# Kernel optimization log

Measured on AMD Instinct MI355X. Metric: run time of the kernel, lower is better.

Reference implementation:

```python
import jax, jax.numpy as jnp
import numpy as np

N = 20000
E = 640000
IN_CH = 256
HID = 128
OUT_CH = 64
HEADS = 8
C1 = HID // HEADS   # 16 per-head dim, layer 1 (concat)
C2 = OUT_CH         # 64 per-head dim, layer 2 (head mean)
NEG_SLOPE = 0.2


def gat_conv(x, edge_index, W, a_src, a_dst, b, concat):
    """PyG GATConv (no self loops, eval mode / no dropout).
    W: [F_in, H*C], a_src/a_dst: [H, C], b: [H*C] or [C]."""
    H, C = a_src.shape
    h = (x @ W).reshape(-1, H, C)                      # [N, H, C]
    s_src = jnp.einsum('nhc,hc->nh', h, a_src)         # [N, H]
    s_dst = jnp.einsum('nhc,hc->nh', h, a_dst)         # [N, H]
    src, dst = edge_index[0], edge_index[1]
    e = jax.nn.leaky_relu(s_src[src] + s_dst[dst], NEG_SLOPE)  # [E, H]
    # segment softmax over incoming edges of each destination node
    m = jax.ops.segment_max(e, dst, num_segments=N)    # [N, H] (-inf for isolated)
    p = jnp.exp(e - m[dst])                            # [E, H]
    z = jax.ops.segment_sum(p, dst, num_segments=N)    # [N, H]
    alpha = p / z[dst]                                 # [E, H]
    out = jax.ops.segment_sum(h[src] * alpha[..., None], dst, num_segments=N)  # [N,H,C]
    out = out.reshape(-1, H * C) if concat else out.mean(axis=1)
    return out + b


def hetero_layer(x, edge_indices, Ws, a_srcs, a_dsts, bs, concat):
    # HeteroConv(aggr='mean') over edge types targeting 'user'
    outs = [gat_conv(x, edge_indices[t], Ws[t], a_srcs[t], a_dsts[t], bs[t], concat)
            for t in range(len(edge_indices))]
    return sum(outs) / len(outs)


def setup_inputs() -> dict:
    key = jax.random.key(0)
    ks = jax.random.split(key, 16)
    g = 0.1
    return {
        'x': jax.random.normal(ks[0], (N, IN_CH), dtype=jnp.float32),
        'edge_index_a': jax.random.randint(ks[1], (2, E), 0, N, dtype=jnp.int32).astype(jnp.int64),
        'edge_index_b': jax.random.randint(ks[2], (2, E), 0, N, dtype=jnp.int32).astype(jnp.int64),
        # layer 1 params, stacked over 2 edge types
        'W1': jax.random.normal(ks[3], (2, IN_CH, HEADS * C1), dtype=jnp.float32) * g,
        'a1_src': jax.random.normal(ks[4], (2, HEADS, C1), dtype=jnp.float32) * g,
        'a1_dst': jax.random.normal(ks[5], (2, HEADS, C1), dtype=jnp.float32) * g,
        'b1': jnp.zeros((2, HEADS * C1), dtype=jnp.float32),
        # layer 2 params
        'W2': jax.random.normal(ks[6], (2, HID, HEADS * C2), dtype=jnp.float32) * g,
        'a2_src': jax.random.normal(ks[7], (2, HEADS, C2), dtype=jnp.float32) * g,
        'a2_dst': jax.random.normal(ks[8], (2, HEADS, C2), dtype=jnp.float32) * g,
        'b2': jnp.zeros((2, C2), dtype=jnp.float32),
        # classifier
        'Wc1': jax.random.normal(ks[9], (OUT_CH, 32), dtype=jnp.float32) * g,
        'bc1': jnp.zeros((32,), dtype=jnp.float32),
        'Wc2': jax.random.normal(ks[10], (32, 2), dtype=jnp.float32) * g,
        'bc2': jnp.zeros((2,), dtype=jnp.float32),
    }


def reference(x, edge_index_a, edge_index_b, W1, a1_src, a1_dst, b1,
              W2, a2_src, a2_dst, b2, Wc1, bc1, Wc2, bc2):
    eis = [edge_index_a, edge_index_b]
    h = hetero_layer(x, eis, W1, a1_src, a1_dst, b1, concat=True)   # [N, 128]
    h = jax.nn.elu(h)  # (dropout is identity in eval mode)
    h = hetero_layer(h, eis, W2, a2_src, a2_dst, b2, concat=False)  # [N, 64]
    h = jax.nn.elu(h)
    logits = jax.nn.relu(h @ Wc1 + bc1) @ Wc2 + bc2                 # [N, 2]
    return logits
```

## Files before the change

### kernel.cpp

```cpp
#include <hip/hip_runtime.h>
#include <hip/hip_bf16.h>
#include <math.h>

#define NN 20000
#define EE 640000
#define NB 157
#define BCAP 5120
#define NBLK 160
#define CHNK 4000

typedef float v2f __attribute__((ext_vector_type(2)));

__device__ __forceinline__ void wave_fence() {
  __builtin_amdgcn_wave_barrier();
  asm volatile("s_waitcnt lgkmcnt(0)" ::: "memory");
  __builtin_amdgcn_wave_barrier();
}

__device__ __forceinline__ unsigned pack_bf2(float a, float b) {
  __hip_bfloat162 h2 = __float22bfloat162_rn(make_float2(a, b));
  return *(unsigned*)&h2;
}
__device__ __forceinline__ float2 unpack_bf2(unsigned v) {
  float2 r;
  unsigned lo = v << 16, hi = v & 0xffff0000u;
  r.x = __uint_as_float(lo);
  r.y = __uint_as_float(hi);
  return r;
}

__global__ __launch_bounds__(256) void bin_k(const int* __restrict__ ea,
                                             const int* __restrict__ eb,
                                             int* __restrict__ gcnt,
                                             int* __restrict__ bbuf) {
  int t = blockIdx.y;
  const int* ei = t ? eb : ea;
  int tid = threadIdx.x;
  __shared__ int lh[NB], lbase[NB];
  if (tid < NB) lh[tid] = 0;
  __syncthreads();
  int e0 = blockIdx.x * CHNK;
  int e1 = min(e0 + CHNK, EE);
  int myb[16], myr[16], myv[16];
#pragma unroll
  for (int i = 0; i < 16; ++i) {
    int e = e0 + tid + i * 256;
    if (e < e1) {
      int s = ei[e], d = ei[EE + e];
      int b = d >> 7;
      myb[i] = b;
      myv[i] = (s << 7) | (d & 127);
      myr[i] = atomicAdd(&lh[b], 1);
    } else {
      myb[i] = -1;
    }
  }
  __syncthreads();
  if (tid < NB) {
    int c = lh[tid];
    lbase[tid] = c ? atomicAdd(&gcnt[t * NB + tid], c) : 0;
  }
  __syncthreads();
#pragma unroll
  for (int i = 0; i < 16; ++i) {
    int b = myb[i];
    if (b >= 0) {
      int pos = lbase[b] + myr[i];
      if (pos < BCAP) bbuf[((size_t)t * NB + b) * BCAP + pos] = myv[i];
    }
  }
}

__global__ __launch_bounds__(512) void bscan_k(const int* __restrict__ gcnt,
                                               int* __restrict__ bstart) {
  __shared__ int buf[512];
  int tid = threadIdx.x;
  int t = tid >> 8, b = tid & 255;
  int val = (b < NB) ? gcnt[t * NB + b] : 0;
  buf[tid] = val;
  __syncthreads();
  for (int s = 1; s < 256; s <<= 1) {
    int x = ((tid & 255) >= s) ? buf[tid - s] : 0;
    __syncthreads();
    buf[tid] += x;
    __syncthreads();
  }
  if (b < NB) bstart[t * NB + b] = buf[tid] - val;
}

__global__ __launch_bounds__(256) void build_k(const int* __restrict__ gcnt,
                                               const int* __restrict__ bstart,
                                               const int* __restrict__ bbuf,
                                               int* __restrict__ rowptr,
                                               int* __restrict__ csr) {
  int b = blockIdx.x, t = blockIdx.y;
  int cnt = gcnt[t * NB + b];
  int start = bstart[t * NB + b];
  int n0 = b << 7;
  int nlocal = min(128, NN - n0);
  int tid = threadIdx.x;
  __shared__ int arr[128], lcur[128];
  if (tid < 128) arr[tid] = 0;
  __syncthreads();
  const int* ebuf = bbuf + ((size_t)t * NB + b) * BCAP;
  for (int i = tid; i < cnt; i += 256) atomicAdd(&arr[ebuf[i] & 127], 1);
  __syncthreads();
  int deg = (tid < 128) ? arr[tid] : 0;
  for (int s = 1; s < 128; s <<= 1) {
    int x = (tid < 128 && tid >= s) ? arr[tid - s] : 0;
    __syncthreads();
    if (tid < 128) arr[tid] += x;
    __syncthreads();
  }
  if (tid < nlocal) {
    int incl = arr[tid];
    rowptr[t * (NN + 1) + n0 + tid + 1] = start + incl;
    lcur[tid] = start + incl - deg;
  }
  if (b == 0 && tid == 0) rowptr[t * (NN + 1)] = 0;
  __syncthreads();
  for (int i = tid; i < cnt; i += 256) {
    int v = ebuf[i];
    int pos = atomicAdd(&lcur[v & 127], 1);
    csr[(size_t)t * EE + pos] = v >> 7;
  }
}

template <int NT, int BM, int BN, int BK, int TM, int TN>
__global__ __launch_bounds__(NT) void sgemm_k(const float* __restrict__ A,
                                              const float* __restrict__ B,
                                              float* __restrict__ C, int M, int N, int K,
                                              long long Abs, long long Bbs, long long Cbs,
                                              unsigned* __restrict__ Cb, long long Cbb) {
  A += blockIdx.z * Abs; B += blockIdx.z * Bbs; C += blockIdx.z * Cbs;
  if (Cb) Cb += blockIdx.z * Cbb;
  const int bm = blockIdx.x * BM, bn = blockIdx.y * BN;
  __shared__ float As[BK][BM + 4];
  __shared__ float Bs[BK][BN + 4];
  int tid = threadIdx.x;
  constexpr int TX = BN / TN;
  int tx = tid % TX, ty = tid / TX;
  float acc[TM][TN] = {};
  for (int k0 = 0; k0 < K; k0 += BK) {
#pragma unroll
    for (int i = 0; i < (BM * BK) / (NT * 4); ++i) {
      int idx = tid + i * NT;
      int row = idx / (BK / 4), kq = idx % (BK / 4);
      float4 v = make_float4(0.f, 0.f, 0.f, 0.f);
      int gr = bm + row;
      if (gr < M) v = *(const float4*)&A[(size_t)gr * K + k0 + kq * 4];
      As[kq * 4 + 0][row] = v.x; As[kq * 4 + 1][row] = v.y;
      As[kq * 4 + 2][row] = v.z; As[kq * 4 + 3][row] = v.w;
    }
#pragma unroll
    for (int i = 0; i < (BK * BN) / (NT * 4); ++i) {
      int idx = tid + i * NT;
      int row = idx / (BN / 4), cq = idx % (BN / 4);
      *(float4*)&Bs[row][cq * 4] = *(const float4*)&B[(size_t)(k0 + row) * N + bn + cq * 4];
    }
    __syncthreads();
#pragma unroll
    for (int k = 0; k < BK; ++k) {
      float a[TM], b[TN];
#pragma unroll
      for (int i = 0; i < TM; i += 4) *(float4*)&a[i] = *(float4*)&As[k][ty * TM + i];
#pragma unroll
      for (int j = 0; j < TN; j += 4) *(float4*)&b[j] = *(float4*)&Bs[k][tx * TN + j];
#pragma unroll
      for (int i = 0; i < TM; ++i)
#pragma unroll
        for (int j = 0; j < TN; ++j) acc[i][j] += a[i] * b[j];
    }
    __syncthreads();
  }
#pragma unroll
  for (int i = 0; i < TM; ++i) {
    int gr = bm + ty * TM + i;
    if (gr < M) {
#pragma unroll
      for (int j = 0; j < TN; j += 4)
        *(float4*)&C[(size_t)gr * N + bn + tx * TN + j] = *(float4*)&acc[i][j];
      if (Cb) {
#pragma unroll
        for (int j = 0; j < TN; j += 2)
          Cb[(size_t)gr * (N >> 1) + ((bn + tx * TN + j) >> 1)] = pack_bf2(acc[i][j], acc[i][j + 1]);
      }
    }
  }
}

template <int NT, int BM, int BK, int TM, int TN, int KC>
__global__ __launch_bounds__(NT) void sgemm_splitk_k(const unsigned* __restrict__ Ap,
                                                     const float* __restrict__ B,
                                                     float* __restrict__ P, int M, int K) {
  const int N = 64;
  int t = blockIdx.z;
  Ap += (size_t)t * M * (K >> 1);
  B += (size_t)t * 65536;
  P += ((size_t)t * 4 + blockIdx.y) * M * N;
  const int bm = blockIdx.x * BM;
  const int k0base = blockIdx.y * KC;
  __shared__ float As[BK][BM + 4];
  __shared__ float Bs[BK][N + 4];
  int tid = threadIdx.x;
  constexpr int TX = N / TN;
  int tx = tid % TX, ty = tid / TX;
  float acc[TM][TN] = {};
  for (int k0 = k0base; k0 < k0base + KC; k0 += BK) {
    {
      int row = tid >> 2, q = tid & 3;
      int gr = bm + row;
      uint4 u = make_uint4(0u, 0u, 0u, 0u);
      if (gr < M) u = *(const uint4*)&Ap[(size_t)gr * (K >> 1) + (k0 >> 1) + q * 4];
      float2 f0 = unpack_bf2(u.x), f1 = unpack_bf2(u.y);
      float2 f2 = unpack_bf2(u.z), f3 = unpack_bf2(u.w);
      int kl = q * 8;
      As[kl + 0][row] = f0.x; As[kl + 1][row] = f0.y;
      As[kl + 2][row] = f1.x; As[kl + 3][row] = f1.y;
      As[kl + 4][row] = f2.x; As[kl + 5][row] = f2.y;
      As[kl + 6][row] = f3.x; As[kl + 7][row] = f3.y;
    }
#pragma unroll
    for (int i = 0; i < (BK * N) / (NT * 4); ++i) {
      int idx = tid + i * NT;
      int row = idx / (N / 4), cq = idx % (N / 4);
      *(float4*)&Bs[row][cq * 4] = *(const float4*)&B[(size_t)(k0 + row) * N + cq * 4];
    }
    __syncthreads();
#pragma unroll
    for (int k = 0; k < BK; ++k) {
      float a[TM], b[TN];
#pragma unroll
      for (int i = 0; i < TM; i += 4) *(float4*)&a[i] = *(float4*)&As[k][ty * TM + i];
#pragma unroll
      for (int j = 0; j < TN; j += 4) *(float4*)&b[j] = *(float4*)&Bs[k][tx * TN + j];
#pragma unroll
      for (int i = 0; i < TM; ++i)
#pragma unroll
        for (int j = 0; j < TN; ++j) acc[i][j] += a[i] * b[j];
    }
    __syncthreads();
  }
#pragma unroll
  for (int i = 0; i < TM; ++i) {
    int gr = bm + ty * TM + i;
    if (gr < M) {
#pragma unroll
      for (int j = 0; j < TN; j += 4)
        *(float4*)&P[(size_t)gr * N + tx * TN + j] = *(float4*)&acc[i][j];
    }
  }
}

template <int C>
__global__ void score_k(const float* __restrict__ hf, const float* __restrict__ as_,
                        const float* __restrict__ ad_, float* __restrict__ ss,
                        float* __restrict__ sd) {
  int idx = blockIdx.x * 256 + threadIdx.x;
  if (idx >= 2 * NN * 8) return;
  int t = idx / (NN * 8), r = idx % (NN * 8), n = r / 8, hh = r % 8;
  const int HC = 8 * C;
  const float* hrow = hf + (size_t)t * NN * HC + (size_t)n * HC + hh * C;
  const float* a1 = as_ + t * HC + hh * C;
  const float* a2 = ad_ + t * HC + hh * C;
  float s1 = 0.f, s2 = 0.f;
#pragma unroll
  for (int c = 0; c < C; c += 4) {
    float4 f = *(const float4*)&hrow[c];
    float4 u = *(const float4*)&a1[c];
    float4 w = *(const float4*)&a2[c];
    s1 += f.x * u.x + f.y * u.y + f.z * u.z + f.w * u.w;
    s2 += f.x * w.x + f.y * w.y + f.z * w.z + f.w * w.w;
  }
  ss[idx] = s1; sd[idx] = s2;
}

__device__ __forceinline__ float lrelu(float v) { return v > 0.f ? v : 0.2f * v; }

__global__ __launch_bounds__(256) void aggw1_k(const int* __restrict__ rowptr,
                                               const int* __restrict__ csr,
                                               const float* __restrict__ ssrc,
                                               const float* __restrict__ sdst,
                                               const unsigned* __restrict__ hb,
                                               float* __restrict__ out) {
  int t = blockIdx.y;
  rowptr += t * (NN + 1); csr += (size_t)t * EE;
  ssrc += (size_t)t * NN * 8; sdst += (size_t)t * NN * 8;
  hb += (size_t)t * NN * 64; out += (size_t)t * NN * 128;
  int tid = threadIdx.x, w = tid >> 6, lane = tid & 63;
  int n = blockIdx.x * 4 + w;
  int row = rowptr[n], end = rowptr[n + 1];
  __shared__ int sidx[4][64];
  __shared__ float sexp[4][64][8];
  float4 sda = *(const float4*)&sdst[(size_t)n * 8];
  float4 sdb = *(const float4*)&sdst[(size_t)n * 8 + 4];
  float za_x = 0.f, za_y = 0.f, za_z = 0.f, za_w = 0.f;
  float zb_x = 0.f, zb_y = 0.f, zb_z = 0.f, zb_w = 0.f;
  int hme = lane >> 3;
  v2f acc = {0.f, 0.f};
  for (int base = row; base < end; base += 64) {
    int cnt = min(64, end - base);
    if (lane < cnt) {
      int s = csr[base + lane];
      sidx[w][lane] = s;
      float4 pa = *(const float4*)&ssrc[(size_t)s * 8];
      float4 pb = *(const float4*)&ssrc[(size_t)s * 8 + 4];
      float4 ea, eb;
      ea.x = __expf(lrelu(pa.x + sda.x)); ea.y = __expf(lrelu(pa.y + sda.y));
      ea.z = __expf(lrelu(pa.z + sda.z)); ea.w = __expf(lrelu(pa.w + sda.w));
      eb.x = __expf(lrelu(pb.x + sdb.x)); eb.y = __expf(lrelu(pb.y + sdb.y));
      eb.z = __expf(lrelu(pb.z + sdb.z)); eb.w = __expf(lrelu(pb.w + sdb.w));
      za_x += ea.x; za_y += ea.y; za_z += ea.z; za_w += ea.w;
      zb_x += eb.x; zb_y += eb.y; zb_z += eb.z; zb_w += eb.w;
      *(float4*)&sexp[w][lane][0] = ea;
      *(float4*)&sexp[w][lane][4] = eb;
    }
    wave_fence();
    for (int e = 0; e < cnt; ++e) {
      int s = sidx[w][e];
      float a = sexp[w][e][hme];
      float2 vf = unpack_bf2(hb[(size_t)s * 64 + lane]);
      v2f v = {vf.x, vf.y};
      acc += a * v;
    }
    wave_fence();
  }
#pragma unroll
  for (int off = 32; off; off >>= 1) {
    za_x += __shfl_xor(za_x, off); za_y += __shfl_xor(za_y, off);
    za_z += __shfl_xor(za_z, off); za_w += __shfl_xor(za_w, off);
    zb_x += __shfl_xor(zb_x, off); zb_y += __shfl_xor(zb_y, off);
    zb_z += __shfl_xor(zb_z, off); zb_w += __shfl_xor(zb_w, off);
  }
  float zh[8] = {za_x, za_y, za_z, za_w, zb_x, zb_y, zb_z, zb_w};
  float z = zh[hme];
  float iz = z > 0.f ? 1.f / z : 0.f;
  *(float2*)&out[(size_t)n * 128 + lane * 2] = make_float2(acc.x * iz, acc.y * iz);
}

__global__ void combine1_k(const float* __restrict__ oa, const float* __restrict__ ob,
                           const float* __restrict__ b1, float* __restrict__ hmid,
                           unsigned* __restrict__ hmidb) {
  int idx = blockIdx.x * 256 + threadIdx.x;
  if (idx >= NN * 64) return;
  int n = idx >> 6, j2 = idx & 63, j = j2 * 2;
  float2 va = *(const float2*)&oa[(size_t)n * 128 + j];
  float2 vb = *(const float2*)&ob[(size_t)n * 128 + j];
  float vx = 0.5f * ((va.x + b1[j]) + (vb.x + b1[128 + j]));
  float vy = 0.5f * ((va.y + b1[j + 1]) + (vb.y + b1[128 + j + 1]));
  vx = vx > 0.f ? vx : (__expf(vx) - 1.f);
  vy = vy > 0.f ? vy : (__expf(vy) - 1.f);
  *(float2*)&hmid[(size_t)n * 128 + j] = make_float2(vx, vy);
  hmidb[idx] = pack_bf2(vx, vy);
}

__global__ void fold2_k(const float* __restrict__ W2, const float* __restrict__ a2s,
                        const float* __restrict__ a2d, float* __restrict__ wsf,
                        float* __restrict__ wdf) {
  int idx = blockIdx.x * 256 + threadIdx.x;
  if (idx >= 2048) return;
  int t = idx >> 10, r = idx & 1023, hh = r >> 7, k = r & 127;
  const float* wrow = W2 + (size_t)t * 65536 + (size_t)k * 512 + hh * 64;
  const float* as = a2s + t * 512 + hh * 64;
  const float* ad = a2d + t * 512 + hh * 64;
  float s1 = 0.f, s2 = 0.f;
  for (int c = 0; c < 64; ++c) { s1 += wrow[c] * as[c]; s2 += wrow[c] * ad[c]; }
  wsf[idx] = s1; wdf[idx] = s2;
}

__global__ void foldB_k(const float* __restrict__ W2, float* __restrict__ Bmat) {
  int idx = blockIdx.x * 256 + threadIdx.x;
  if (idx >= 131072) return;
  int t = idx >> 16, r = idx & 65535, rowr = r >> 6, c = r & 63;
  int hh = rowr >> 7, k = rowr & 127;
  Bmat[idx] = 0.125f * W2[(size_t)t * 65536 + (size_t)k * 512 + hh * 64 + c];
}

__global__ void score2_k(const float* __restrict__ hmid, const float* __restrict__ wsf,
                         const float* __restrict__ wdf, float* __restrict__ ss,
                         float* __restrict__ sdo) {
  int idx = blockIdx.x * 256 + threadIdx.x;
  if (idx >= NN * 8) return;
  int n = idx >> 3, hh = idx & 7;
  const float* hm = hmid + (size_t)n * 128;
  const float* w0s = wsf + (size_t)hh * 128;
  const float* w0d = wdf + (size_t)hh * 128;
  const float* w1s = wsf + (size_t)(8 + hh) * 128;
  const float* w1d = wdf + (size_t)(8 + hh) * 128;
  float s0s = 0.f, s0d = 0.f, s1s = 0.f, s1d = 0.f;
#pragma unroll
  for (int c = 0; c < 128; c += 4) {
    float4 f = *(const float4*)&hm[c];
    float4 a = *(const float4*)&w0s[c];
    float4 b = *(const float4*)&w0d[c];
    float4 u = *(const float4*)&w1s[c];
    float4 v = *(const float4*)&w1d[c];
    s0s += f.x * a.x + f.y * a.y + f.z * a.z + f.w * a.w;
    s0d += f.x * b.x + f.y * b.y + f.z * b.z + f.w * b.w;
    s1s += f.x * u.x + f.y * u.y + f.z * u.z + f.w * u.w;
    s1d += f.x * v.x + f.y * v.y + f.z * v.z + f.w * v.w;
  }
  ss[idx] = s0s; sdo[idx] = s0d;
  ss[NN * 8 + idx] = s1s; sdo[NN * 8 + idx] = s1d;
}

__global__ __launch_bounds__(256) void aggw2_k(const int* __restrict__ rowptr,
                                               const int* __restrict__ csr,
                                               const float* __restrict__ ssrc,
                                               const float* __restrict__ sdst,
                                               const unsigned* __restrict__ hmidb,
                                               unsigned* __restrict__ aggp) {
  int t = blockIdx.y;
  rowptr += t * (NN + 1); csr += (size_t)t * EE;
  ssrc += (size_t)t * NN * 8; sdst += (size_t)t * NN * 8;
  aggp += (size_t)t * NN * 512;
  int tid = threadIdx.x, w = tid >> 6, lane = tid & 63;
  int n = blockIdx.x * 4 + w;
  int row = rowptr[n], end = rowptr[n + 1];
  __shared__ int sidx[4][64];
  __shared__ float sexp[4][64][8];
  float4 sda = *(const float4*)&sdst[(size_t)n * 8];
  float4 sdb = *(const float4*)&sdst[(size_t)n * 8 + 4];
  float za_x = 0.f, za_y = 0.f, za_z = 0.f, za_w = 0.f;
  float zb_x = 0.f, zb_y = 0.f, zb_z = 0.f, zb_w = 0.f;
  v2f acc[8];
#pragma unroll
  for (int i = 0; i < 8; ++i) acc[i] = (v2f){0.f, 0.f};
  for (int base = row; base < end; base += 64) {
    int cnt = min(64, end - base);
    if (lane < cnt) {
      int s = csr[base + lane];
      sidx[w][lane] = s;
      float4 pa = *(const float4*)&ssrc[(size_t)s * 8];
      float4 pb = *(const float4*)&ssrc[(size_t)s * 8 + 4];
      float4 ea, eb;
      ea.x = __expf(lrelu(pa.x + sda.x)); ea.y = __expf(lrelu(pa.y + sda.y));
      ea.z = __expf(lrelu(pa.z + sda.z)); ea.w = __expf(lrelu(pa.w + sda.w));
      eb.x = __expf(lrelu(pb.x + sdb.x)); eb.y = __expf(lrelu(pb.y + sdb.y));
      eb.z = __expf(lrelu(pb.z + sdb.z)); eb.w = __expf(lrelu(pb.w + sdb.w));
      za_x += ea.x; za_y += ea.y; za_z += ea.z; za_w += ea.w;
      zb_x += eb.x; zb_y += eb.y; zb_z += eb.z; zb_w += eb.w;
      *(float4*)&sexp[w][lane][0] = ea;
      *(float4*)&sexp[w][lane][4] = eb;
    }
    wave_fence();
    for (int e = 0; e < cnt; ++e) {
      int s = sidx[w][e];
      unsigned uv = hmidb[(size_t)s * 64 + lane];
      float4 ea = *(const float4*)&sexp[w][e][0];
      float4 eb = *(const float4*)&sexp[w][e][4];
      float2 vf = unpack_bf2(uv);
      v2f v = {vf.x, vf.y};
      acc[0] += ea.x * v;
      acc[1] += ea.y * v;
      acc[2] += ea.z * v;
      acc[3] += ea.w * v;
      acc[4] += eb.x * v;
      acc[5] += eb.y * v;
      acc[6] += eb.z * v;
      acc[7] += eb.w * v;
    }
    wave_fence();
  }
#pragma unroll
  for (int off = 32; off; off >>= 1) {
    za_x += __shfl_xor(za_x, off); za_y += __shfl_xor(za_y, off);
    za_z += __shfl_xor(za_z, off); za_w += __shfl_xor(za_w, off);
    zb_x += __shfl_xor(zb_x, off); zb_y += __shfl_xor(zb_y, off);
    zb_z += __shfl_xor(zb_z, off); zb_w += __shfl_xor(zb_w, off);
  }
  float zh[8] = {za_x, za_y, za_z, za_w, zb_x, zb_y, zb_z, zb_w};
#pragma unroll
  for (int i = 0; i < 8; ++i) {
    float z = zh[i];
    float iz = z > 0.f ? 1.f / z : 0.f;
    aggp[(size_t)n * 512 + i * 64 + lane] = pack_bf2(acc[i].x * iz, acc[i].y * iz);
  }
}

__global__ void combine2p_k(const float* __restrict__ P, const float* __restrict__ b2,
                            float* __restrict__ feat) {
  int idx = blockIdx.x * 256 + threadIdx.x;
  if (idx >= NN * 16) return;
  int n = idx >> 4, j = (idx & 15) * 4;
  const size_t SZ = (size_t)NN * 64;
  size_t o = (size_t)n * 64 + j;
  float4 sa = make_float4(0.f, 0.f, 0.f, 0.f), sb = sa;
#pragma unroll
  for (int k = 0; k < 4; ++k) {
    float4 va = *(const float4*)&P[k * SZ + o];
    float4 vb = *(const float4*)&P[(4 + k) * SZ + o];
    sa.x += va.x; sa.y += va.y; sa.z += va.z; sa.w += va.w;
    sb.x += vb.x; sb.y += vb.y; sb.z += vb.z; sb.w += vb.w;
  }
  float4 ba = *(const float4*)&b2[j];
  float4 bb = *(const float4*)&b2[64 + j];
  float4 v;
  v.x = 0.5f * ((sa.x + ba.x) + (sb.x + bb.x));
  v.y = 0.5f * ((sa.y + ba.y) + (sb.y + bb.y));
  v.z = 0.5f * ((sa.z + ba.z) + (sb.z + bb.z));
  v.w = 0.5f * ((sa.w + ba.w) + (sb.w + bb.w));
  v.x = v.x > 0.f ? v.x : (__expf(v.x) - 1.f);
  v.y = v.y > 0.f ? v.y : (__expf(v.y) - 1.f);
  v.z = v.z > 0.f ? v.z : (__expf(v.z) - 1.f);
  v.w = v.w > 0.f ? v.w : (__expf(v.w) - 1.f);
  *(float4*)&feat[o] = v;
}

__global__ __launch_bounds__(256) void cls_k(const float* __restrict__ feat,
                                             const float* __restrict__ Wc1,
                                             const float* __restrict__ bc1,
                                             const float* __restrict__ Wc2,
                                             const float* __restrict__ bc2,
                                             float* __restrict__ out) {
  __shared__ float w1[64 * 32];
  __shared__ float w2[64];
  __shared__ float b1s[32], b2s[2];
  __shared__ float fs[8 * 64];
  __shared__ float hs[8 * 32];
  int tid = threadIdx.x;
  for (int i = tid; i < 2048; i += 256) w1[i] = Wc1[i];
  if (tid < 64) w2[tid] = Wc2[tid];
  if (tid < 32) b1s[tid] = bc1[tid];
  if (tid < 2) b2s[tid] = bc2[tid];
  int nbase = blockIdx.x * 8;
  for (int i = tid; i < 512; i += 256) fs[i] = feat[(size_t)nbase * 64 + i];
  __syncthreads();
  int local = tid >> 5, tt = tid & 31;
  const float* f = fs + local * 64;
  float acc = b1s[tt];
#pragma unroll
  for (int c = 0; c < 64; ++c) acc += f[c] * w1[c * 32 + tt];
  hs[local * 32 + tt] = fmaxf(acc, 0.f);
  __syncthreads();
  if (tid < 16) {
    int l = tid >> 1, j = tid & 1;
    float o = b2s[j];
#pragma unroll
    for (int i = 0; i < 32; ++i) o += hs[l * 32 + i] * w2[i * 2 + j];
    out[(size_t)(nbase + l) * 2 + j] = o;
  }
}

extern "C" void kernel_launch(void* const* d_in, const int* in_sizes, int n_in,
                              void* d_out, int out_size, void* d_ws, size_t ws_size,
                              hipStream_t stream) {
  const float* x   = (const float*)d_in[0];
  const int* eia   = (const int*)d_in[1];
  const int* eib   = (const int*)d_in[2];
  const float* W1  = (const float*)d_in[3];
  const float* a1s = (const float*)d_in[4];
  const float* a1d = (const float*)d_in[5];
  const float* b1  = (const float*)d_in[6];
  const float* W2  = (const float*)d_in[7];
  const float* a2s = (const float*)d_in[8];
  const float* a2d = (const float*)d_in[9];
  const float* b2  = (const float*)d_in[10];
  const float* Wc1 = (const float*)d_in[11];
  const float* bc1 = (const float*)d_in[12];
  const float* Wc2 = (const float*)d_in[13];
  const float* bc2 = (const float*)d_in[14];
  float* out = (float*)d_out;

  char* ws = (char*)d_ws;
  size_t off = 0;
  auto alloc = [&](size_t bytes) -> char* {
    char* p = ws + off;
    off += (bytes + 255) & ~(size_t)255;
    return p;
  };
  int* gcnt       = (int*)alloc((size_t)2 * NB * 4);
  int* bstart     = (int*)alloc((size_t)2 * NB * 4);
  int* bbuf       = (int*)alloc((size_t)2 * NB * BCAP * 4);
  int* rowptr     = (int*)alloc((size_t)2 * (NN + 1) * 4);
  int* csr        = (int*)alloc((size_t)2 * EE * 4);
  float* h1       = (float*)alloc((size_t)2 * NN * 128 * 4);
  unsigned* h1b   = (unsigned*)alloc((size_t)2 * NN * 64 * 4);
  float* s1s      = (float*)alloc((size_t)2 * NN * 8 * 4);
  float* s1d      = (float*)alloc((size_t)2 * NN * 8 * 4);
  float* o1       = (float*)alloc((size_t)2 * NN * 128 * 4);
  float* hmid     = (float*)alloc((size_t)NN * 128 * 4);
  unsigned* hmidb = (unsigned*)alloc((size_t)NN * 64 * 4);
  float* wsf      = (float*)alloc((size_t)2048 * 4);
  float* wdf      = (float*)alloc((size_t)2048 * 4);
  float* Bmat     = (float*)alloc((size_t)131072 * 4);
  float* s2s      = (float*)alloc((size_t)2 * NN * 8 * 4);
  float* s2d      = (float*)alloc((size_t)2 * NN * 8 * 4);
  unsigned* aggp  = (unsigned*)alloc((size_t)2 * NN * 512 * 4);
  float* pbuf     = (float*)alloc((size_t)8 * NN * 64 * 4);
  float* feat     = (float*)alloc((size_t)NN * 64 * 4);

  hipMemsetAsync(gcnt, 0, (size_t)2 * NB * 4, stream);
  bin_k<<<dim3(NBLK, 2), 256, 0, stream>>>(eia, eib, gcnt, bbuf);
  bscan_k<<<1, 512, 0, stream>>>(gcnt, bstart);
  build_k<<<dim3(NB, 2), 256, 0, stream>>>(gcnt, bstart, bbuf, rowptr, csr);

  fold2_k<<<8, 256, 0, stream>>>(W2, a2s, a2d, wsf, wdf);
  foldB_k<<<512, 256, 0, stream>>>(W2, Bmat);

  sgemm_k<256, 64, 64, 32, 4, 4><<<dim3((NN + 63) / 64, 2, 2), 256, 0, stream>>>(
      x, W1, h1, NN, 128, 256, 0LL, 256LL * 128, (long long)NN * 128, h1b, (long long)NN * 64);
  score_k<16><<<(2 * NN * 8 + 255) / 256, 256, 0, stream>>>(h1, a1s, a1d, s1s, s1d);
  aggw1_k<<<dim3(NN / 4, 2), 256, 0, stream>>>(rowptr, csr, s1s, s1d, h1b, o1);
  combine1_k<<<(NN * 64 + 255) / 256, 256, 0, stream>>>(o1, o1 + (size_t)NN * 128, b1, hmid, hmidb);

  score2_k<<<(NN * 8 + 255) / 256, 256, 0, stream>>>(hmid, wsf, wdf, s2s, s2d);
  aggw2_k<<<dim3(NN / 4, 2), 256, 0, stream>>>(rowptr, csr, s2s, s2d, hmidb, aggp);
  sgemm_splitk_k<256, 64, 32, 4, 4, 256><<<dim3((NN + 63) / 64, 4, 2), 256, 0, stream>>>(
      aggp, Bmat, pbuf, NN, 1024);
  combine2p_k<<<(NN * 16 + 255) / 256, 256, 0, stream>>>(pbuf, b2, feat);

  cls_k<<<NN / 8, 256, 0, stream>>>(feat, Wc1, bc1, Wc2, bc2, out);
}
```

Baseline: 445.5 us.

## Replace split-K fp32 layer-2 GEMM with fused bf16 MFMA GEMM plus epilogue

Replaces the split-K scalar fp32 GEMM over the aggregated layer-2 features, and its separate combine kernel, with one kernel that uses bf16 16x16x32 MFMA instructions. It reduces over both edge types and the full K inside the kernel, then applies bias, head-mean and ELU in the epilogue. The weight fold now writes a transposed bf16-packed matrix so MFMA B fragments load directly from global memory. This removes the 8-way partial-sum buffer and its extra pass, at the cost of bf16 weights and no shared-memory staging for B, so each wave re-reads B from cache.

```diff
diff --git a/kernel.cpp b/kernel.cpp
--- a/kernel.cpp
+++ b/kernel.cpp
@@ -10,6 +10,8 @@
 #define CHNK 4000
 
 typedef float v2f __attribute__((ext_vector_type(2)));
+typedef __attribute__((ext_vector_type(8))) short bf16x8;
+typedef __attribute__((ext_vector_type(4))) float f32x4;
 
 __device__ __forceinline__ void wave_fence() {
   __builtin_amdgcn_wave_barrier();
@@ -185,69 +187,6 @@
         for (int j = 0; j < TN; j += 2)
           Cb[(size_t)gr * (N >> 1) + ((bn + tx * TN + j) >> 1)] = pack_bf2(acc[i][j], acc[i][j + 1]);
       }
-    }
-  }
-}
-
-template <int NT, int BM, int BK, int TM, int TN, int KC>
-__global__ __launch_bounds__(NT) void sgemm_splitk_k(const unsigned* __restrict__ Ap,
-                                                     const float* __restrict__ B,
-                                                     float* __restrict__ P, int M, int K) {
-  const int N = 64;
-  int t = blockIdx.z;
-  Ap += (size_t)t * M * (K >> 1);
-  B += (size_t)t * 65536;
-  P += ((size_t)t * 4 + blockIdx.y) * M * N;
-  const int bm = blockIdx.x * BM;
-  const int k0base = blockIdx.y * KC;
-  __shared__ float As[BK][BM + 4];
-  __shared__ float Bs[BK][N + 4];
-  int tid = threadIdx.x;
-  constexpr int TX = N / TN;
-  int tx = tid % TX, ty = tid / TX;
-  float acc[TM][TN] = {};
-  for (int k0 = k0base; k0 < k0base + KC; k0 += BK) {
-    {
-      int row = tid >> 2, q = tid & 3;
-      int gr = bm + row;
-      uint4 u = make_uint4(0u, 0u, 0u, 0u);
-      if (gr < M) u = *(const uint4*)&Ap[(size_t)gr * (K >> 1) + (k0 >> 1) + q * 4];
-      float2 f0 = unpack_bf2(u.x), f1 = unpack_bf2(u.y);
-      float2 f2 = unpack_bf2(u.z), f3 = unpack_bf2(u.w);
-      int kl = q * 8;
-      As[kl + 0][row] = f0.x; As[kl + 1][row] = f0.y;
-      As[kl + 2][row] = f1.x; As[kl + 3][row] = f1.y;
-      As[kl + 4][row] = f2.x; As[kl + 5][row] = f2.y;
-      As[kl + 6][row] = f3.x; As[kl + 7][row] = f3.y;
-    }
-#pragma unroll
-    for (int i = 0; i < (BK * N) / (NT * 4); ++i) {
-      int idx = tid + i * NT;
-      int row = idx / (N / 4), cq = idx % (N / 4);
-      *(float4*)&Bs[row][cq * 4] = *(const float4*)&B[(size_t)(k0 + row) * N + cq * 4];
-    }
-    __syncthreads();
-#pragma unroll
-    for (int k = 0; k < BK; ++k) {
-      float a[TM], b[TN];
-#pragma unroll
-      for (int i = 0; i < TM; i += 4) *(float4*)&a[i] = *(float4*)&As[k][ty * TM + i];
-#pragma unroll
-      for (int j = 0; j < TN; j += 4) *(float4*)&b[j] = *(float4*)&Bs[k][tx * TN + j];
-#pragma unroll
-      for (int i = 0; i < TM; ++i)
-#pragma unroll
-        for (int j = 0; j < TN; ++j) acc[i][j] += a[i] * b[j];
-    }
-    __syncthreads();
-  }
-#pragma unroll
-  for (int i = 0; i < TM; ++i) {
-    int gr = bm + ty * TM + i;
-    if (gr < M) {
-#pragma unroll
-      for (int j = 0; j < TN; j += 4)
-        *(float4*)&P[(size_t)gr * N + tx * TN + j] = *(float4*)&acc[i][j];
     }
   }
 }
@@ -368,12 +307,16 @@
   wsf[idx] = s1; wdf[idx] = s2;
 }
 
-__global__ void foldB_k(const float* __restrict__ W2, float* __restrict__ Bmat) {
+__global__ void foldBT_k(const float* __restrict__ W2, unsigned* __restrict__ BTp) {
   int idx = blockIdx.x * 256 + threadIdx.x;
-  if (idx >= 131072) return;
-  int t = idx >> 16, r = idx & 65535, rowr = r >> 6, c = r & 63;
-  int hh = rowr >> 7, k = rowr & 127;
-  Bmat[idx] = 0.125f * W2[(size_t)t * 65536 + (size_t)k * 512 + hh * 64 + c];
+  if (idx >= 65536) return;
+  int t = idx >> 15, r = idx & 32767, c = r >> 9, kw = r & 511;
+  int K0 = kw * 2, K1 = K0 + 1;
+  int hh0 = K0 >> 7, kk0 = K0 & 127;
+  int hh1 = K1 >> 7, kk1 = K1 & 127;
+  float v0 = 0.125f * W2[(size_t)t * 65536 + (size_t)kk0 * 512 + hh0 * 64 + c];
+  float v1 = 0.125f * W2[(size_t)t * 65536 + (size_t)kk1 * 512 + hh1 * 64 + c];
+  BTp[idx] = pack_bf2(v0, v1);
 }
 
 __global__ void score2_k(const float* __restrict__ hmid, const float* __restrict__ wsf,
@@ -478,33 +421,48 @@
   }
 }
 
-__global__ void combine2p_k(const float* __restrict__ P, const float* __restrict__ b2,
-                            float* __restrict__ feat) {
-  int idx = blockIdx.x * 256 + threadIdx.x;
-  if (idx >= NN * 16) return;
-  int n = idx >> 4, j = (idx & 15) * 4;
-  const size_t SZ = (size_t)NN * 64;
-  size_t o = (size_t)n * 64 + j;
-  float4 sa = make_float4(0.f, 0.f, 0.f, 0.f), sb = sa;
-#pragma unroll
-  for (int k = 0; k < 4; ++k) {
-    float4 va = *(const float4*)&P[k * SZ + o];
-    float4 vb = *(const float4*)&P[(4 + k) * SZ + o];
-    sa.x += va.x; sa.y += va.y; sa.z += va.z; sa.w += va.w;
-    sb.x += vb.x; sb.y += vb.y; sb.z += vb.z; sb.w += vb.w;
-  }
-  float4 ba = *(const float4*)&b2[j];
-  float4 bb = *(const float4*)&b2[64 + j];
-  float4 v;
-  v.x = 0.5f * ((sa.x + ba.x) + (sb.x + bb.x));
-  v.y = 0.5f * ((sa.y + ba.y) + (sb.y + bb.y));
-  v.z = 0.5f * ((sa.z + ba.z) + (sb.z + bb.z));
-  v.w = 0.5f * ((sa.w + ba.w) + (sb.w + bb.w));
-  v.x = v.x > 0.f ? v.x : (__expf(v.x) - 1.f);
-  v.y = v.y > 0.f ? v.y : (__expf(v.y) - 1.f);
-  v.z = v.z > 0.f ? v.z : (__expf(v.z) - 1.f);
-  v.w = v.w > 0.f ? v.w : (__expf(v.w) - 1.f);
-  *(float4*)&feat[o] = v;
+__global__ __launch_bounds__(256) void gemm2_k(const unsigned* __restrict__ Ap,
+                                               const unsigned* __restrict__ BT,
+                                               const float* __restrict__ b2,
+                                               float* __restrict__ feat) {
+  int tid = threadIdx.x, w = tid >> 6, l = tid & 63;
+  int lr = l & 15, lg = l >> 4;
+  int rowbase = blockIdx.x * 64 + w * 16;
+  int arow = rowbase + lr;
+  if (arow > NN - 1) arow = NN - 1;
+  f32x4 acc0 = {0.f, 0.f, 0.f, 0.f}, acc1 = acc0, acc2 = acc0, acc3 = acc0;
+#pragma unroll
+  for (int t = 0; t < 2; ++t) {
+    const unsigned* ap = Ap + (size_t)t * NN * 512 + (size_t)arow * 512 + lg * 4;
+    const unsigned* bp = BT + t * 32768 + lr * 512 + lg * 4;
+    for (int kw = 0; kw < 512; kw += 16) {
+      uint4 av = *(const uint4*)(ap + kw);
+      uint4 bv0 = *(const uint4*)(bp + kw);
+      uint4 bv1 = *(const uint4*)(bp + 16 * 512 + kw);
+      uint4 bv2 = *(const uint4*)(bp + 32 * 512 + kw);
+      uint4 bv3 = *(const uint4*)(bp + 48 * 512 + kw);
+      bf16x8 af = *(const bf16x8*)&av;
+      acc0 = __builtin_amdgcn_mfma_f32_16x16x32_bf16(af, *(const bf16x8*)&bv0, acc0, 0, 0, 0);
+      acc1 = __builtin_amdgcn_mfma_f32_16x16x32_bf16(af, *(const bf16x8*)&bv1, acc1, 0, 0, 0);
+      acc2 = __builtin_amdgcn_mfma_f32_16x16x32_bf16(af, *(const bf16x8*)&bv2, acc2, 0, 0, 0);
+      acc3 = __builtin_amdgcn_mfma_f32_16x16x32_bf16(af, *(const bf16x8*)&bv3, acc3, 0, 0, 0);
+    }
+  }
+  f32x4 accs[4] = {acc0, acc1, acc2, acc3};
+#pragma unroll
+  for (int ct = 0; ct < 4; ++ct) {
+    int col = ct * 16 + lr;
+    float bsum = b2[col] + b2[64 + col];
+#pragma unroll
+    for (int r = 0; r < 4; ++r) {
+      int row = rowbase + lg * 4 + r;
+      if (row < NN) {
+        float v = 0.5f * (accs[ct][r] + bsum);
+        v = v > 0.f ? v : (__expf(v) - 1.f);
+        feat[(size_t)row * 64 + col] = v;
+      }
+    }
+  }
 }
 
 __global__ __launch_bounds__(256) void cls_k(const float* __restrict__ feat,
@@ -583,11 +541,10 @@
   unsigned* hmidb = (unsigned*)alloc((size_t)NN * 64 * 4);
   float* wsf      = (float*)alloc((size_t)2048 * 4);
   float* wdf      = (float*)alloc((size_t)2048 * 4);
-  float* Bmat     = (float*)alloc((size_t)131072 * 4);
+  unsigned* BTp   = (unsigned*)alloc((size_t)65536 * 4);
   float* s2s      = (float*)alloc((size_t)2 * NN * 8 * 4);
   float* s2d      = (float*)alloc((size_t)2 * NN * 8 * 4);
   unsigned* aggp  = (unsigned*)alloc((size_t)2 * NN * 512 * 4);
-  float* pbuf     = (float*)alloc((size_t)8 * NN * 64 * 4);
   float* feat     = (float*)alloc((size_t)NN * 64 * 4);
 
   hipMemsetAsync(gcnt, 0, (size_t)2 * NB * 4, stream);
@@ -596,7 +553,7 @@
   build_k<<<dim3(NB, 2), 256, 0, stream>>>(gcnt, bstart, bbuf, rowptr, csr);
 
   fold2_k<<<8, 256, 0, stream>>>(W2, a2s, a2d, wsf, wdf);
-  foldB_k<<<512, 256, 0, stream>>>(W2, Bmat);
+  foldBT_k<<<256, 256, 0, stream>>>(W2, BTp);
 
   sgemm_k<256, 64, 64, 32, 4, 4><<<dim3((NN + 63) / 64, 2, 2), 256, 0, stream>>>(
       x, W1, h1, NN, 128, 256, 0LL, 256LL * 128, (long long)NN * 128, h1b, (long long)NN * 64);
@@ -606,9 +563,7 @@
 
   score2_k<<<(NN * 8 + 255) / 256, 256, 0, stream>>>(hmid, wsf, wdf, s2s, s2d);
   aggw2_k<<<dim3(NN / 4, 2), 256, 0, stream>>>(rowptr, csr, s2s, s2d, hmidb, aggp);
-  sgemm_splitk_k<256, 64, 32, 4, 4, 256><<<dim3((NN + 63) / 64, 4, 2), 256, 0, stream>>>(
-      aggp, Bmat, pbuf, NN, 1024);
-  combine2p_k<<<(NN * 16 + 255) / 256, 256, 0, stream>>>(pbuf, b2, feat);
+  gemm2_k<<<(NN + 63) / 64, 256, 0, stream>>>(aggp, BTp, b2, feat);
 
   cls_k<<<NN / 8, 256, 0, stream>>>(feat, Wc1, bc1, Wc2, bc2, out);
 }
```

Result: no change. 444.3 us (-0.3%).
